# Optimization experiments

Measured on AMD Instinct MI355X. Metric: run time of the kernel, lower is better.

The kernel has to match this reference:

```python
import jax, jax.numpy as jnp
import numpy as np

B, N, HIDDEN = 4, 2048, 512
N_HEADS, HEAD_DIM = 8, 64
N_CANCER = 32
SCALE = float(np.sqrt(HEAD_DIM))


def setup_inputs() -> dict:
    key = jax.random.key(0)
    ks = jax.random.split(key, 16)
    s = 0.02
    return {
        "x": jax.random.normal(ks[0], (B, N, HIDDEN), dtype=jnp.float32),
        "cancer_type": jax.random.randint(ks[1], (B,), 0, N_CANCER, dtype=jnp.int64),
        "attn_mask": jnp.zeros((B, N), dtype=bool),
        "wq": jax.random.normal(ks[2], (HIDDEN, HIDDEN), dtype=jnp.float32) * s,
        "bq": jnp.zeros((HIDDEN,), dtype=jnp.float32),
        "wk": jax.random.normal(ks[3], (HIDDEN, HIDDEN), dtype=jnp.float32) * s,
        "bk": jnp.zeros((HIDDEN,), dtype=jnp.float32),
        "wv": jax.random.normal(ks[4], (HIDDEN, HIDDEN), dtype=jnp.float32) * s,
        "bv": jnp.zeros((HIDDEN,), dtype=jnp.float32),
        "wo": jax.random.normal(ks[5], (HIDDEN, HIDDEN), dtype=jnp.float32) * s,
        "bo": jnp.zeros((HIDDEN,), dtype=jnp.float32),
        "bias_emb": jax.random.normal(ks[6], (N_CANCER, N_HEADS), dtype=jnp.float32) * s,
        "keymod_emb": jax.random.normal(ks[7], (N_CANCER, HIDDEN), dtype=jnp.float32) * s,
    }


def reference(x, cancer_type, attn_mask, wq, bq, wk, bk, wv, bv, wo, bo, bias_emb, keymod_emb):
    Bc, Nc, _ = x.shape
    # projections (torch Linear: x @ W.T + b), split heads -> (B, H, N, D)
    def split_heads(t):
        return t.reshape(Bc, Nc, N_HEADS, HEAD_DIM).transpose(0, 2, 1, 3)
    q = split_heads(x @ wq.T + bq)
    k = split_heads(x @ wk.T + bk)
    v = split_heads(x @ wv.T + bv)
    # cancer-conditioned key offset: (B, H, 1, D)
    ct_key = keymod_emb[cancer_type].reshape(Bc, 1, N_HEADS, HEAD_DIM).transpose(0, 2, 1, 3)
    k = k + ct_key
    # scores + per-head cancer bias
    attn = jnp.einsum("bhnd,bhmd->bhnm", q, k) / SCALE
    ct_bias = bias_emb[cancer_type]  # (B, H)
    attn = attn + ct_bias[:, :, None, None]
    attn = jnp.where(attn_mask[:, None, None, :], -jnp.inf, attn)
    attn = jax.nn.softmax(attn, axis=-1)
    # dropout is identity in eval mode
    out = jnp.einsum("bhnm,bhmd->bhnd", attn, v)
    out = out.transpose(0, 2, 1, 3).reshape(Bc, Nc, HIDDEN)
    return out @ wo.T + bo
```

## Files before the change

### kernel.cpp

```cpp
#include <hip/hip_runtime.h>

#define B_    4
#define N_    2048
#define HID   512
#define NH    8
#define HD    64
#define TOK   (B_ * N_)
#define LOG2E 1.4426950408889634f

typedef __attribute__((ext_vector_type(8))) short short8;
typedef __attribute__((ext_vector_type(4))) float f32x4;
typedef unsigned short u16;

static __device__ __forceinline__ u16 f2bf(float f) {
    unsigned int u = __builtin_bit_cast(unsigned int, f);
    u += 0x7FFFu + ((u >> 16) & 1u);
    return (u16)(u >> 16);
}
static __device__ __forceinline__ unsigned pktrunc(float a, float b) {
    return __builtin_amdgcn_perm(__builtin_bit_cast(unsigned, b),
                                 __builtin_bit_cast(unsigned, a), 0x07060302u);
}

__global__ __launch_bounds__(256) void cvt_all(
    const float* __restrict__ x,
    const float* __restrict__ w0, const float* __restrict__ w1,
    const float* __restrict__ w2, const float* __restrict__ w3,
    u16* __restrict__ xb,
    u16* __restrict__ d0, u16* __restrict__ d1,
    u16* __restrict__ d2, u16* __restrict__ d3)
{
    const int bid = blockIdx.x;
    const float* s;
    u16* d;
    int off;
    if (bid < 4096) { s = x; d = xb; off = bid; }
    else {
        const int t = (bid - 4096) >> 8;
        off = (bid - 4096) & 255;
        s = t == 0 ? w0 : t == 1 ? w1 : t == 2 ? w2 : w3;
        d = t == 0 ? d0 : t == 1 ? d1 : t == 2 ? d2 : d3;
    }
    const int i = off * 1024 + threadIdx.x * 4;
    const float4 v = *(const float4*)&s[i];
    ushort4 o;
    o.x = f2bf(v.x); o.y = f2bf(v.y); o.z = f2bf(v.z); o.w = f2bf(v.w);
    *(ushort4*)&d[i] = o;
}

__global__ __launch_bounds__(256) void gemm_mfma(
    const u16* __restrict__ A,
    const u16* __restrict__ W0, const u16* __restrict__ W1, const u16* __restrict__ W2,
    const float* __restrict__ bias0, const float* __restrict__ bias1, const float* __restrict__ bias2,
    void* __restrict__ C0, void* __restrict__ C1, void* __restrict__ C2,
    int qkv)
{
    const int z = blockIdx.z;
    const u16*   W    = z == 0 ? W0 : z == 1 ? W1 : W2;
    const float* bias = z == 0 ? bias0 : z == 1 ? bias1 : bias2;

    __shared__ u16 sh[2 * 128 * 40];
    u16 (*As)[40] = (u16(*)[40])sh;
    u16 (*Bs)[40] = (u16(*)[40])(sh + 128 * 40);
    u16 (*St)[72] = (u16(*)[72])sh;

    const int tid  = threadIdx.x;
    const int row0 = blockIdx.x * 128, col0 = blockIdx.y * 128;
    const int w    = tid >> 6, lane = tid & 63;
    const int wr   = w >> 1, wc = w & 1;
    const int t16  = lane & 15, q4 = lane >> 4;

    const int sm = tid >> 2, sc = (tid & 3) * 8;

    f32x4 acc[4][4];
    #pragma unroll
    for (int mt = 0; mt < 4; ++mt)
        #pragma unroll
        for (int nt = 0; nt < 4; ++nt)
            acc[mt][nt] = (f32x4){0.f, 0.f, 0.f, 0.f};

    short8 apre[2], wpre[2];
    #pragma unroll
    for (int p = 0; p < 2; ++p) {
        const int m = sm + 64 * p;
        apre[p] = *(const short8*)&A[(size_t)(row0 + m) * HID + sc];
        wpre[p] = *(const short8*)&W[(size_t)(col0 + m) * HID + sc];
    }

    for (int k0 = 0; k0 < HID; k0 += 32) {
        __syncthreads();
        #pragma unroll
        for (int p = 0; p < 2; ++p) {
            const int m = sm + 64 * p;
            *(short8*)&As[m][sc] = apre[p];
            *(short8*)&Bs[m][sc] = wpre[p];
        }
        __syncthreads();

        if (k0 + 32 < HID) {
            #pragma unroll
            for (int p = 0; p < 2; ++p) {
                const int m = sm + 64 * p;
                apre[p] = *(const short8*)&A[(size_t)(row0 + m) * HID + k0 + 32 + sc];
                wpre[p] = *(const short8*)&W[(size_t)(col0 + m) * HID + k0 + 32 + sc];
            }
        }

        short8 af[4], bf[4];
        #pragma unroll
        for (int mt = 0; mt < 4; ++mt)
            af[mt] = *(const short8*)&As[wr * 64 + mt * 16 + t16][q4 * 8];
        #pragma unroll
        for (int nt = 0; nt < 4; ++nt)
            bf[nt] = *(const short8*)&Bs[wc * 64 + nt * 16 + t16][q4 * 8];
        #pragma unroll
        for (int mt = 0; mt < 4; ++mt)
            #pragma unroll
            for (int nt = 0; nt < 4; ++nt)
                acc[mt][nt] = __builtin_amdgcn_mfma_f32_16x16x32_bf16(
                    af[mt], bf[nt], acc[mt][nt], 0, 0, 0);
    }

    if (!qkv) {
        #pragma unroll
        for (int nt = 0; nt < 4; ++nt) {
            const int j = col0 + wc * 64 + nt * 16 + t16;
            const float bv = bias[j];
            #pragma unroll
            for (int mt = 0; mt < 4; ++mt)
                #pragma unroll
                for (int r = 0; r < 4; ++r) {
                    const int i = row0 + wr * 64 + mt * 16 + q4 * 4 + r;
                    ((float*)C0)[(size_t)i * HID + j] = acc[mt][nt][r] + bv;
                }
        }
    } else if (z < 2) {
        const float qscale = (z == 0) ? 0.125f * LOG2E : 1.0f;
        u16* C = (u16*)(z == 0 ? C0 : C1);
        #pragma unroll
        for (int nt = 0; nt < 4; ++nt) {
            const int j = col0 + wc * 64 + nt * 16 + t16;
            const float bv = bias[j];
            const int h = j >> 6, d = j & 63;
            #pragma unroll
            for (int mt = 0; mt < 4; ++mt)
                #pragma unroll
                for (int r = 0; r < 4; ++r) {
                    const int i = row0 + wr * 64 + mt * 16 + q4 * 4 + r;
                    const int b = i >> 11, n = i & (N_ - 1);
                    C[(((size_t)(b * NH + h)) * N_ + n) * HD + d] =
                        f2bf((acc[mt][nt][r] + bv) * qscale);
                }
        }
    } else {
        u16* Vt = (u16*)C2;
        const int b = row0 >> 11;
        #pragma unroll
        for (int p = 0; p < 2; ++p) {
            __syncthreads();
            if (wr == p) {
                #pragma unroll
                for (int nt = 0; nt < 4; ++nt) {
                    const int jp = wc * 64 + nt * 16 + t16;
                    const float bv = bias[col0 + jp];
                    #pragma unroll
                    for (int mt = 0; mt < 4; ++mt) {
                        const float v0 = acc[mt][nt][0] + bv;
                        const float v1 = acc[mt][nt][1] + bv;
                        const float v2 = acc[mt][nt][2] + bv;
                        const float v3 = acc[mt][nt][3] + bv;
                        uint2 pk;
                        pk.x = pktrunc(v0, v1);
                        pk.y = pktrunc(v2, v3);
                        *(uint2*)&St[jp][mt * 16 + q4 * 4] = pk;
                    }
                }
            }
            __syncthreads();
            const int nb = (row0 & (N_ - 1)) + p * 64;
            #pragma unroll
            for (int it = 0; it < 2; ++it) {
                const int task = tid + it * 256;
                const int jp = task >> 2, qc = task & 3;
                u16 v[16];
                #pragma unroll
                for (int e = 0; e < 16; ++e) {
                    const int np = qc * 16 + e;
                    const int n  = ((np & 3) << 4) | (np >> 2);
                    v[e] = St[jp][n];
                }
                const int j = col0 + jp, h = j >> 6, d = j & 63;
                u16* dst = &Vt[(((size_t)(b * NH + h)) * HD + d) * N_ + nb + qc * 16];
                *(short8*)(dst)     = *(const short8*)&v[0];
                *(short8*)(dst + 8) = *(const short8*)&v[8];
            }
        }
    }
}

__global__ __launch_bounds__(128) void flash_mfma(
    const u16* __restrict__ Qg, const u16* __restrict__ Kg,
    const u16* __restrict__ Vtg, const unsigned char* __restrict__ msk,
    u16* __restrict__ AOg)
{
    __shared__ u16 Ks[64][72];
    __shared__ u16 Vts[64][72];
    __shared__ u16 Ps[2][32][72];
    __shared__ unsigned Mnd[N_ / 64][32];

    const int tid = threadIdx.x;
    const int w = tid >> 6, lane = tid & 63;
    const int t16 = lane & 15, q4 = lane >> 4;
    const int bh = blockIdx.y, b = bh >> 3, h = bh & 7;
    const int qrow0 = blockIdx.x * 64;

    const size_t hb = (size_t)bh * N_ * HD;
    const u16* Qh  = Qg + hb;
    const u16* Kh  = Kg + hb;
    const u16* Vth = Vtg + hb;
    const unsigned char* mrow = msk + b * N_;

    #pragma unroll
    for (int it = 0; it < 8; ++it) {
        const int e = tid + it * 128;
        const int kt = e >> 5, sl = e & 31;
        const int tt = sl >> 1, wd = sl & 1;
        const int k0 = kt * 64 + wd * 32 + tt;
        const unsigned lo = mrow[k0]      ? 0u : 0x0000FFFFu;
        const unsigned hi = mrow[k0 + 16] ? 0u : 0xFFFF0000u;
        Mnd[kt][sl] = lo | hi;
    }

    short8 qf[2][2];
    #pragma unroll
    for (int mt = 0; mt < 2; ++mt)
        #pragma unroll
        for (int kk = 0; kk < 2; ++kk)
            qf[mt][kk] = *(const short8*)
                &Qh[(size_t)(qrow0 + w * 32 + mt * 16 + t16) * HD + kk * 32 + q4 * 8];

    const short8 ones8 = {0x3F80, 0x3F80, 0x3F80, 0x3F80,
                          0x3F80, 0x3F80, 0x3F80, 0x3F80};

    f32x4 o[2][4], ls[2];
    #pragma unroll
    for (int mt = 0; mt < 2; ++mt) {
        #pragma unroll
        for (int nt = 0; nt < 4; ++nt) o[mt][nt] = (f32x4){0.f, 0.f, 0.f, 0.f};
        ls[mt] = (f32x4){0.f, 0.f, 0.f, 0.f};
    }

    const int sr = tid >> 1, scc = (tid & 1) * 32;

    short8 kreg[4], vreg[4];
    #pragma unroll
    for (int i = 0; i < 4; ++i) {
        kreg[i] = *(const short8*)&Kh[(size_t)sr * HD + scc + i * 8];
        vreg[i] = *(const short8*)&Vth[(size_t)sr * N_ + scc + i * 8];
    }

    for (int kt = 0; kt < N_ / 64; ++kt) {
        const int kb = kt * 64;
        __syncthreads();
        #pragma unroll
        for (int i = 0; i < 4; ++i) {
            *(short8*)&Ks[sr][scc + i * 8]  = kreg[i];
            *(short8*)&Vts[sr][scc + i * 8] = vreg[i];
        }
        __syncthreads();

        if (kt + 1 < N_ / 64) {
            const int kb2 = kb + 64;
            #pragma unroll
            for (int i = 0; i < 4; ++i) {
                kreg[i] = *(const short8*)&Kh[(size_t)(kb2 + sr) * HD + scc + i * 8];
                vreg[i] = *(const short8*)&Vth[(size_t)sr * N_ + kb2 + scc + i * 8];
            }
        }

        f32x4 s[2][4];
        #pragma unroll
        for (int mt = 0; mt < 2; ++mt)
            #pragma unroll
            for (int f = 0; f < 4; ++f)
                s[mt][f] = (f32x4){0.f, 0.f, 0.f, 0.f};
        #pragma unroll
        for (int f = 0; f < 4; ++f) {
            #pragma unroll
            for (int kk = 0; kk < 2; ++kk) {
                const short8 kf = *(const short8*)&Ks[f * 16 + t16][kk * 32 + q4 * 8];
                #pragma unroll
                for (int mt = 0; mt < 2; ++mt)
                    s[mt][f] = __builtin_amdgcn_mfma_f32_16x16x32_bf16(
                        qf[mt][kk], kf, s[mt][f], 0, 0, 0);
            }
        }

        const uint2 mnd = *(const uint2*)&Mnd[kt][t16 * 2];

        #pragma unroll
        for (int mt = 0; mt < 2; ++mt) {
            #pragma unroll
            for (int r = 0; r < 4; ++r) {
                const float e0 = __builtin_amdgcn_exp2f(s[mt][0][r]);
                const float e1 = __builtin_amdgcn_exp2f(s[mt][1][r]);
                const float e2 = __builtin_amdgcn_exp2f(s[mt][2][r]);
                const float e3 = __builtin_amdgcn_exp2f(s[mt][3][r]);
                uint2 pk;
                pk.x = pktrunc(e0, e1) & mnd.x;
                pk.y = pktrunc(e2, e3) & mnd.y;
                *(uint2*)&Ps[w][mt * 16 + q4 * 4 + r][t16 * 4] = pk;
            }
        }

        short8 pf[2][2];
        #pragma unroll
        for (int mt = 0; mt < 2; ++mt)
            #pragma unroll
            for (int kk = 0; kk < 2; ++kk)
                pf[mt][kk] = *(const short8*)&Ps[w][mt * 16 + t16][kk * 32 + q4 * 8];
        #pragma unroll
        for (int mt = 0; mt < 2; ++mt)
            #pragma unroll
            for (int kk = 0; kk < 2; ++kk)
                ls[mt] = __builtin_amdgcn_mfma_f32_16x16x32_bf16(
                    pf[mt][kk], ones8, ls[mt], 0, 0, 0);
        #pragma unroll
        for (int nt = 0; nt < 4; ++nt) {
            #pragma unroll
            for (int kk = 0; kk < 2; ++kk) {
                const short8 vf = *(const short8*)&Vts[nt * 16 + t16][kk * 32 + q4 * 8];
                #pragma unroll
                for (int mt = 0; mt < 2; ++mt)
                    o[mt][nt] = __builtin_amdgcn_mfma_f32_16x16x32_bf16(
                        pf[mt][kk], vf, o[mt][nt], 0, 0, 0);
            }
        }
    }

    #pragma unroll
    for (int mt = 0; mt < 2; ++mt) {
        #pragma unroll
        for (int r = 0; r < 4; ++r) {
            const float inv = 1.f / ls[mt][r];
            const int n = qrow0 + w * 32 + mt * 16 + q4 * 4 + r;
            #pragma unroll
            for (int nt = 0; nt < 4; ++nt)
                AOg[((size_t)(b * N_ + n)) * HID + h * 64 + nt * 16 + t16] =
                    f2bf(o[mt][nt][r] * inv);
        }
    }
}

extern "C" void kernel_launch(void* const* d_in, const int* in_sizes, int n_in,
                              void* d_out, int out_size, void* d_ws, size_t ws_size,
                              hipStream_t stream) {
    const float* x  = (const float*)d_in[0];
    const unsigned char* mask = (const unsigned char*)d_in[2];
    const float* wq = (const float*)d_in[3];
    const float* bq = (const float*)d_in[4];
    const float* wk = (const float*)d_in[5];
    const float* bk = (const float*)d_in[6];
    const float* wv = (const float*)d_in[7];
    const float* bv = (const float*)d_in[8];
    const float* wo = (const float*)d_in[9];
    const float* bo = (const float*)d_in[10];

    char* ws = (char*)d_ws;
    u16* xb  = (u16*)(ws);
    u16* wqb = (u16*)(ws + (8u << 20));
    u16* wkb = (u16*)(ws + (8u << 20) + (512u << 10));
    u16* wvb = (u16*)(ws + (8u << 20) + (1024u << 10));
    u16* wob = (u16*)(ws + (8u << 20) + (1536u << 10));
    u16* Qg  = (u16*)(ws + (10u << 20));
    u16* Kg  = (u16*)(ws + (18u << 20));
    u16* Vtg = (u16*)(ws + (26u << 20));
    u16* AOg = xb;

    cvt_all<<<5120, 256, 0, stream>>>(x, wq, wk, wv, wo, xb, wqb, wkb, wvb, wob);

    gemm_mfma<<<dim3(TOK / 128, HID / 128, 3), 256, 0, stream>>>(
        xb, wqb, wkb, wvb, bq, bk, bv, Qg, Kg, Vtg, 1);

    flash_mfma<<<dim3(N_ / 64, B_ * NH), 128, 0, stream>>>(Qg, Kg, Vtg, mask, AOg);

    gemm_mfma<<<dim3(TOK / 128, HID / 128, 1), 256, 0, stream>>>(
        AOg, wob, wob, wob, bo, bo, bo, d_out, d_out, d_out, 0);
}
```

Measured before the change: 195.1 us.

## Use direct global-to-LDS DMA with double-buffered swizzled tiles in GEMM and flash

Replaces the register-staged global→LDS copies in both the projection GEMM and the flash-attention kernel with global_load_lds DMA into double-buffered LDS tiles that use an XOR swizzle. This removes one barrier per iteration and the VGPR round trip, so the loads overlap with the MFMA work. The flash kernel also grows to 256 threads covering 128 query rows, which halves how often each K/V tile is loaded per query. The price is more LDS per block and a dependence on the DMA's per-lane placement matching the swizzle. With only one barrier there is a risk of a race where the next prefetch overwrites a buffer other waves are still reading, unless the DMA wait semantics cover it.

```diff
diff --git a/kernel.cpp b/kernel.cpp
--- a/kernel.cpp
+++ b/kernel.cpp
@@ -20,6 +20,13 @@
 static __device__ __forceinline__ unsigned pktrunc(float a, float b) {
     return __builtin_amdgcn_perm(__builtin_bit_cast(unsigned, b),
                                  __builtin_bit_cast(unsigned, a), 0x07060302u);
+}
+
+static __device__ __forceinline__ void dma16(const void* g, void* l) {
+    __builtin_amdgcn_global_load_lds(
+        (const __attribute__((address_space(1))) unsigned int*)(unsigned long long)g,
+        (__attribute__((address_space(3))) unsigned int*)(unsigned int)(unsigned long long)l,
+        16, 0, 0);
 }
 
 __global__ __launch_bounds__(256) void cvt_all(
@@ -59,10 +66,7 @@
     const u16*   W    = z == 0 ? W0 : z == 1 ? W1 : W2;
     const float* bias = z == 0 ? bias0 : z == 1 ? bias1 : bias2;
 
-    __shared__ u16 sh[2 * 128 * 40];
-    u16 (*As)[40] = (u16(*)[40])sh;
-    u16 (*Bs)[40] = (u16(*)[40])(sh + 128 * 40);
-    u16 (*St)[72] = (u16(*)[72])sh;
+    __shared__ u16 ABs[2][2][128 * 32];
 
     const int tid  = threadIdx.x;
     const int row0 = blockIdx.x * 128, col0 = blockIdx.y * 128;
@@ -70,7 +74,8 @@
     const int wr   = w >> 1, wc = w & 1;
     const int t16  = lane & 15, q4 = lane >> 4;
 
-    const int sm = tid >> 2, sc = (tid & 3) * 8;
+    const int dmr  = lane >> 2;
+    const int dmc8 = (lane & 3) ^ ((lane >> 2) & 3) ^ ((lane >> 4) & 3);
 
     f32x4 acc[4][4];
     #pragma unroll
@@ -79,40 +84,32 @@
         for (int nt = 0; nt < 4; ++nt)
             acc[mt][nt] = (f32x4){0.f, 0.f, 0.f, 0.f};
 
-    short8 apre[2], wpre[2];
-    #pragma unroll
-    for (int p = 0; p < 2; ++p) {
-        const int m = sm + 64 * p;
-        apre[p] = *(const short8*)&A[(size_t)(row0 + m) * HID + sc];
-        wpre[p] = *(const short8*)&W[(size_t)(col0 + m) * HID + sc];
-    }
-
-    for (int k0 = 0; k0 < HID; k0 += 32) {
+    #define GEMM_DMA(p, k0)                                                     \
+        _Pragma("unroll")                                                       \
+        for (int i = 0; i < 2; ++i) {                                           \
+            const int c = w * 2 + i;                                            \
+            dma16(&A[(size_t)(row0 + c * 16 + dmr) * HID + (k0) + dmc8 * 8],    \
+                  &ABs[p][0][c * 512]);                                         \
+            dma16(&W[(size_t)(col0 + c * 16 + dmr) * HID + (k0) + dmc8 * 8],    \
+                  &ABs[p][1][c * 512]);                                         \
+        }
+
+    GEMM_DMA(0, 0)
+
+    const int swz = (t16 ^ (t16 >> 2)) & 3;
+
+    for (int it = 0; it < HID / 32; ++it) {
         __syncthreads();
-        #pragma unroll
-        for (int p = 0; p < 2; ++p) {
-            const int m = sm + 64 * p;
-            *(short8*)&As[m][sc] = apre[p];
-            *(short8*)&Bs[m][sc] = wpre[p];
-        }
-        __syncthreads();
-
-        if (k0 + 32 < HID) {
-            #pragma unroll
-            for (int p = 0; p < 2; ++p) {
-                const int m = sm + 64 * p;
-                apre[p] = *(const short8*)&A[(size_t)(row0 + m) * HID + k0 + 32 + sc];
-                wpre[p] = *(const short8*)&W[(size_t)(col0 + m) * HID + k0 + 32 + sc];
-            }
-        }
-
+        if (it + 1 < HID / 32) { GEMM_DMA((it + 1) & 1, (it + 1) * 32) }
+
+        const int p = it & 1;
         short8 af[4], bf[4];
         #pragma unroll
         for (int mt = 0; mt < 4; ++mt)
-            af[mt] = *(const short8*)&As[wr * 64 + mt * 16 + t16][q4 * 8];
+            af[mt] = *(const short8*)&ABs[p][0][(wr * 64 + mt * 16 + t16) * 32 + (q4 ^ swz) * 8];
         #pragma unroll
         for (int nt = 0; nt < 4; ++nt)
-            bf[nt] = *(const short8*)&Bs[wc * 64 + nt * 16 + t16][q4 * 8];
+            bf[nt] = *(const short8*)&ABs[p][1][(wc * 64 + nt * 16 + t16) * 32 + (q4 ^ swz) * 8];
         #pragma unroll
         for (int mt = 0; mt < 4; ++mt)
             #pragma unroll
@@ -154,6 +151,7 @@
         }
     } else {
         u16* Vt = (u16*)C2;
+        u16 (*St)[72] = (u16(*)[72])&ABs[0][0][0];
         const int b = row0 >> 11;
         #pragma unroll
         for (int p = 0; p < 2; ++p) {
@@ -165,13 +163,9 @@
                     const float bv = bias[col0 + jp];
                     #pragma unroll
                     for (int mt = 0; mt < 4; ++mt) {
-                        const float v0 = acc[mt][nt][0] + bv;
-                        const float v1 = acc[mt][nt][1] + bv;
-                        const float v2 = acc[mt][nt][2] + bv;
-                        const float v3 = acc[mt][nt][3] + bv;
                         uint2 pk;
-                        pk.x = pktrunc(v0, v1);
-                        pk.y = pktrunc(v2, v3);
+                        pk.x = pktrunc(acc[mt][nt][0] + bv, acc[mt][nt][1] + bv);
+                        pk.y = pktrunc(acc[mt][nt][2] + bv, acc[mt][nt][3] + bv);
                         *(uint2*)&St[jp][mt * 16 + q4 * 4] = pk;
                     }
                 }
@@ -198,21 +192,21 @@
     }
 }
 
-__global__ __launch_bounds__(128) void flash_mfma(
+__global__ __launch_bounds__(256) void flash_mfma(
     const u16* __restrict__ Qg, const u16* __restrict__ Kg,
     const u16* __restrict__ Vtg, const unsigned char* __restrict__ msk,
     u16* __restrict__ AOg)
 {
-    __shared__ u16 Ks[64][72];
-    __shared__ u16 Vts[64][72];
-    __shared__ u16 Ps[2][32][72];
+    __shared__ u16 KVs[2][2][64 * 64];
+    __shared__ u16 Ps[4][32][72];
     __shared__ unsigned Mnd[N_ / 64][32];
 
     const int tid = threadIdx.x;
     const int w = tid >> 6, lane = tid & 63;
     const int t16 = lane & 15, q4 = lane >> 4;
     const int bh = blockIdx.y, b = bh >> 3, h = bh & 7;
-    const int qrow0 = blockIdx.x * 64;
+    const int qrow0 = blockIdx.x * 128;
+    const int qbase = qrow0 + w * 32;
 
     const size_t hb = (size_t)bh * N_ * HD;
     const u16* Qh  = Qg + hb;
@@ -221,8 +215,8 @@
     const unsigned char* mrow = msk + b * N_;
 
     #pragma unroll
-    for (int it = 0; it < 8; ++it) {
-        const int e = tid + it * 128;
+    for (int it = 0; it < 4; ++it) {
+        const int e = tid + it * 256;
         const int kt = e >> 5, sl = e & 31;
         const int tt = sl >> 1, wd = sl & 1;
         const int k0 = kt * 64 + wd * 32 + tt;
@@ -237,7 +231,7 @@
         #pragma unroll
         for (int kk = 0; kk < 2; ++kk)
             qf[mt][kk] = *(const short8*)
-                &Qh[(size_t)(qrow0 + w * 32 + mt * 16 + t16) * HD + kk * 32 + q4 * 8];
+                &Qh[(size_t)(qbase + mt * 16 + t16) * HD + kk * 32 + q4 * 8];
 
     const short8 ones8 = {0x3F80, 0x3F80, 0x3F80, 0x3F80,
                           0x3F80, 0x3F80, 0x3F80, 0x3F80};
@@ -250,33 +244,27 @@
         ls[mt] = (f32x4){0.f, 0.f, 0.f, 0.f};
     }
 
-    const int sr = tid >> 1, scc = (tid & 1) * 32;
-
-    short8 kreg[4], vreg[4];
-    #pragma unroll
-    for (int i = 0; i < 4; ++i) {
-        kreg[i] = *(const short8*)&Kh[(size_t)sr * HD + scc + i * 8];
-        vreg[i] = *(const short8*)&Vth[(size_t)sr * N_ + scc + i * 8];
-    }
+    const int dmr  = lane >> 3;
+    const int dmc8 = (lane & 7) ^ ((lane >> 3) & 7);
+
+    #define FLASH_DMA(p, kb)                                                    \
+        _Pragma("unroll")                                                       \
+        for (int i = 0; i < 2; ++i) {                                           \
+            const int c = w * 2 + i;                                            \
+            dma16(&Kh[(size_t)((kb) + c * 8 + dmr) * HD + dmc8 * 8],            \
+                  &KVs[p][0][c * 512]);                                         \
+            dma16(&Vth[(size_t)(c * 8 + dmr) * N_ + (kb) + dmc8 * 8],           \
+                  &KVs[p][1][c * 512]);                                         \
+        }
+
+    FLASH_DMA(0, 0)
+
+    const int swz7 = t16 & 7;
 
     for (int kt = 0; kt < N_ / 64; ++kt) {
-        const int kb = kt * 64;
         __syncthreads();
-        #pragma unroll
-        for (int i = 0; i < 4; ++i) {
-            *(short8*)&Ks[sr][scc + i * 8]  = kreg[i];
-            *(short8*)&Vts[sr][scc + i * 8] = vreg[i];
-        }
-        __syncthreads();
-
-        if (kt + 1 < N_ / 64) {
-            const int kb2 = kb + 64;
-            #pragma unroll
-            for (int i = 0; i < 4; ++i) {
-                kreg[i] = *(const short8*)&Kh[(size_t)(kb2 + sr) * HD + scc + i * 8];
-                vreg[i] = *(const short8*)&Vth[(size_t)sr * N_ + kb2 + scc + i * 8];
-            }
-        }
+        if (kt + 1 < N_ / 64) { FLASH_DMA((kt + 1) & 1, (kt + 1) * 64) }
+        const int p = kt & 1;
 
         f32x4 s[2][4];
         #pragma unroll
@@ -288,7 +276,8 @@
         for (int f = 0; f < 4; ++f) {
             #pragma unroll
             for (int kk = 0; kk < 2; ++kk) {
-                const short8 kf = *(const short8*)&Ks[f * 16 + t16][kk * 32 + q4 * 8];
+                const short8 kf = *(const short8*)
+                    &KVs[p][0][(f * 16 + t16) * 64 + ((kk * 4 + q4) ^ swz7) * 8];
                 #pragma unroll
                 for (int mt = 0; mt < 2; ++mt)
                     s[mt][f] = __builtin_amdgcn_mfma_f32_16x16x32_bf16(
@@ -329,7 +318,8 @@
         for (int nt = 0; nt < 4; ++nt) {
             #pragma unroll
             for (int kk = 0; kk < 2; ++kk) {
-                const short8 vf = *(const short8*)&Vts[nt * 16 + t16][kk * 32 + q4 * 8];
+                const short8 vf = *(const short8*)
+                    &KVs[p][1][(nt * 16 + t16) * 64 + ((kk * 4 + q4) ^ swz7) * 8];
                 #pragma unroll
                 for (int mt = 0; mt < 2; ++mt)
                     o[mt][nt] = __builtin_amdgcn_mfma_f32_16x16x32_bf16(
@@ -343,7 +333,7 @@
         #pragma unroll
         for (int r = 0; r < 4; ++r) {
             const float inv = 1.f / ls[mt][r];
-            const int n = qrow0 + w * 32 + mt * 16 + q4 * 4 + r;
+            const int n = qbase + mt * 16 + q4 * 4 + r;
             #pragma unroll
             for (int nt = 0; nt < 4; ++nt)
                 AOg[((size_t)(b * N_ + n)) * HID + h * 64 + nt * 16 + t16] =
@@ -382,7 +372,7 @@
     gemm_mfma<<<dim3(TOK / 128, HID / 128, 3), 256, 0, stream>>>(
         xb, wqb, wkb, wvb, bq, bk, bv, Qg, Kg, Vtg, 1);
 
-    flash_mfma<<<dim3(N_ / 64, B_ * NH), 128, 0, stream>>>(Qg, Kg, Vtg, mask, AOg);
+    flash_mfma<<<dim3(N_ / 128, B_ * NH), 256, 0, stream>>>(Qg, Kg, Vtg, mask, AOg);
 
     gemm_mfma<<<dim3(TOK / 128, HID / 128, 1), 256, 0, stream>>>(
         AOg, wob, wob, wob, bo, bo, bo, d_out, d_out, d_out, 0);
```

New measurement: 178.8 us. 8.4% less time.
